# Optimization experiments

Measured on AMD Instinct MI355X. Metric: run time of the kernel, lower is better.

## Reference

```python
import jax, jax.numpy as jnp
import numpy as np

S, L, E = 64, 256, 768          # sentences, tokens per sentence, BERT hidden
N, P = 4096, 32768              # events, event pairs
C, H, D = 256, 4, 64            # CGE channels, heads, head dim (C = H*D = n_last)
M = 8                           # max event span length
MLP_H = 1024
ITERS = 3                       # max_iteration + 1
RATE = 0.5
BETA_INTRA, BETA_INTER = 0.5, 0.5


def setup_inputs():
    key = jax.random.key(0)
    ks = jax.random.split(key, 16)
    nrm = lambda k, shape, sc: jax.random.normal(k, shape, dtype=jnp.float32) * sc
    event_start = jax.random.randint(ks[2], (N,), 0, L - M)
    span = jax.random.randint(ks[3], (N,), 1, M + 1)
    return {
        "sent_emb": nrm(ks[0], (S, L, E), 1.0),
        "proj_in_W": nrm(ks[7], (E, C), E ** -0.5),
        "proj_in_b": jnp.zeros((C,), jnp.float32),
        "proj_W": nrm(ks[8], (C, C), C ** -0.5),
        "proj_b": jnp.zeros((C,), jnp.float32),
        "att_src_intra": nrm(ks[9], (H, D), D ** -0.5),
        "att_dst_intra": nrm(ks[10], (H, D), D ** -0.5),
        "att_src_inter": nrm(ks[11], (H, D), D ** -0.5),
        "att_dst_inter": nrm(ks[12], (H, D), D ** -0.5),
        "mlp_W1": nrm(ks[13], (C + 2 * E, MLP_H), (C + 2 * E) ** -0.5),
        "mlp_b1": jnp.zeros((MLP_H,), jnp.float32),
        "mlp_W2": nrm(ks[14], (MLP_H, 3), MLP_H ** -0.5),
        "mlp_b2": jnp.zeros((3,), jnp.float32),
        "event_sent": jax.random.randint(ks[1], (N,), 0, S),
        "event_start": event_start,
        "event_end": event_start + span,
        "pair_idx": jax.random.randint(ks[4], (P, 2), 0, N),
        "rel_type": jax.random.randint(ks[5], (P,), 0, 2),
        "target": jax.random.randint(ks[6], (P,), 0, 3),
    }


def _attend(h, src, dst, emask, att_src, att_dst):
    # h: [N,H,D]. Masked graph attention, softmax over incoming edges per dst.
    a = jax.nn.leaky_relu((h[src] * att_src).sum(-1) + (h[dst] * att_dst).sum(-1), 0.2)  # [En,H]
    a = jnp.where(emask[:, None], a, -1e9)
    amax = jnp.maximum(jax.ops.segment_max(a, dst, num_segments=N), -1e9)  # [N,H]
    ex = jnp.exp(a - amax[dst]) * emask[:, None].astype(a.dtype)
    denom = jax.ops.segment_sum(ex, dst, num_segments=N)
    alpha = ex / (denom[dst] + 1e-9)
    out = jax.ops.segment_sum(alpha[:, :, None] * h[src], dst, num_segments=N)  # [N,H,D]
    return out.reshape(N, H * D)


def _forward(sent_emb, proj_in_W, proj_in_b, proj_W, proj_b,
             att_src_intra, att_dst_intra, att_src_inter, att_dst_inter,
             mlp_W1, mlp_b1, mlp_W2, mlp_b2,
             event_sent, event_start, event_end, pair_idx, rel_type, target):
    # extract_event: mean of sentence token embeddings over each event span
    pos = event_start[:, None] + jnp.arange(M)                      # [N,M]
    vmask = (pos < event_end[:, None]).astype(sent_emb.dtype)       # [N,M]
    tok = sent_emb[event_sent[:, None], jnp.clip(pos, 0, L - 1)]    # [N,M,E]
    e_emb = (tok * vmask[..., None]).sum(1) / (event_end - event_start).astype(sent_emb.dtype)[:, None]

    p0, p1 = pair_idx[:, 0], pair_idx[:, 1]
    pair_emb = jnp.concatenate([e_emb[p0], e_emb[p1]], axis=-1)     # [P,2E]
    x = e_emb @ proj_in_W + proj_in_b                               # [N,C]

    self_idx = jnp.arange(N)
    ones_n = jnp.ones((N,), bool)
    src_all = jnp.concatenate([p0, p1])
    dst_all = jnp.concatenate([p1, p0])
    intra2 = jnp.concatenate([rel_type == 0, rel_type == 0])

    loss = jnp.float32(0.0)
    pred = None
    for it in range(ITERS):
        diff = x[p0] - x[p1]                                        # [P,C]
        pre = jnp.concatenate([pair_emb, diff], axis=-1)            # [P,2E+C]
        pred = jax.nn.relu(pre @ mlp_W1 + mlp_b1) @ mlp_W2 + mlp_b2  # [P,3]
        logp = jax.nn.log_softmax(pred, axis=-1)
        loss = loss + (1.0 / (it + 1)) * (-jnp.take_along_axis(logp, target[:, None], axis=1).mean())

        # data-dependent edge construction (masked, fixed-size edge lists)
        psoft = jax.nn.softmax(pred, axis=-1)
        conf = psoft.max(1) > RATE
        parg = psoft.argmax(1)
        m_all = jnp.concatenate([conf & (parg == 1), conf & (parg == 2)])

        h = (x @ proj_W + proj_b).reshape(N, H, D)
        # intra edges + always-on self loops
        src_i = jnp.concatenate([src_all, self_idx])
        dst_i = jnp.concatenate([dst_all, self_idx])
        m_i = jnp.concatenate([m_all & intra2, ones_n])
        out_intra = _attend(h, src_i, dst_i, m_i, att_src_intra, att_dst_intra)
        out_inter = _attend(h, src_all, dst_all, m_all & (~intra2), att_src_inter, att_dst_inter)
        x = BETA_INTRA * out_intra + BETA_INTER * out_inter
    return loss, pred


def reference(sent_emb, proj_in_W, proj_in_b, proj_W, proj_b,
              att_src_intra, att_dst_intra, att_src_inter, att_dst_inter,
              mlp_W1, mlp_b1, mlp_W2, mlp_b2,
              event_sent, event_start, event_end, pair_idx, rel_type, target):
    return _forward(sent_emb, proj_in_W, proj_in_b, proj_W, proj_b,
                    att_src_intra, att_dst_intra, att_src_inter, att_dst_inter,
                    mlp_W1, mlp_b1, mlp_W2, mlp_b2,
                    event_sent, event_start, event_end, pair_idx, rel_type, target)
```

## Files before the change

kernel.cpp:

```cpp
#include <hip/hip_runtime.h>
#include <cstddef>
#include <cstdint>

#define NEV   4096
#define NPAIR 32768
#define NEDGE (2*NPAIR)
#define EDIM  768
#define CDIM  256
#define MLPH  1024
#define LLEN  256

typedef unsigned short u16;
typedef __attribute__((ext_vector_type(8))) short bhalf8;
typedef __attribute__((ext_vector_type(4))) float f32x4;

#define GLOAD_LDS(g, l) __builtin_amdgcn_global_load_lds( \
    (const __attribute__((address_space(1))) unsigned int*)(g), \
    (__attribute__((address_space(3))) unsigned int*)(l), 16, 0, 0)

__device__ inline u16 f2bf(float f) {
  union { float f; unsigned u; } v; v.f = f;
  unsigned r = v.u + 0x7fffu + ((v.u >> 16) & 1u);
  return (u16)(r >> 16);
}
__device__ inline float bf2f(u16 h) {
  union { unsigned u; float f; } v; v.u = ((unsigned)h) << 16; return v.f;
}

__global__ void k_zero(int* __restrict__ deg, int* __restrict__ pdeg,
                       float* __restrict__ out) {
  int i = blockIdx.x * 256 + threadIdx.x;
  if (i < NEV) { deg[i] = 0; pdeg[i] = 0; }
  if (i == 0) out[0] = 0.f;
}

__global__ void k_embed(const float* __restrict__ sent, const int* __restrict__ es,
                        const int* __restrict__ st, const int* __restrict__ en,
                        u16* __restrict__ Ahat) {
  int node = blockIdx.x;
  int s = es[node];
  int a = st[node];
  int span = en[node] - a;
  float fspan = (float)span;
  const float* base = sent + ((size_t)s * LLEN + a) * EDIM;
  for (int d = threadIdx.x; d < EDIM; d += 256) {
    float acc = 0.f;
    for (int m = 0; m < span; ++m) acc += base[(size_t)m * EDIM + d];
    float e = acc / fspan;
    u16 hi = f2bf(e);
    float lo = e - bf2f(hi);
    size_t b = (size_t)node * (3 * EDIM);
    Ahat[b + d] = hi;
    Ahat[b + EDIM + d] = hi;
    Ahat[b + 2 * EDIM + d] = f2bf(lo);
  }
}

__global__ void k_count(const int* __restrict__ pair, int* __restrict__ deg) {
  int e = blockIdx.x * 256 + threadIdx.x;
  if (e >= NEDGE) return;
  int p = (e < NPAIR) ? e : e - NPAIR;
  int dst = (e < NPAIR) ? pair[2 * p + 1] : pair[2 * p];
  atomicAdd(&deg[dst], 1);
}

__global__ void k_scan(const int* __restrict__ deg, int* __restrict__ rowp,
                       int* __restrict__ cursor) {
  __shared__ int part[256];
  int t = threadIdx.x;
  int base = t * 16;
  int sum = 0;
  for (int i = 0; i < 16; ++i) sum += deg[base + i];
  part[t] = sum;
  __syncthreads();
  for (int off = 1; off < 256; off <<= 1) {
    int v = (t >= off) ? part[t - off] : 0;
    __syncthreads();
    part[t] += v;
    __syncthreads();
  }
  int run = (t == 0) ? 0 : part[t - 1];
  for (int i = 0; i < 16; ++i) {
    rowp[base + i] = run;
    cursor[base + i] = 0;
    run += deg[base + i];
  }
  if (t == 255) rowp[NEV] = run;
}

__global__ void k_scatter(const int* __restrict__ pair, const int* __restrict__ rowp,
                          int* __restrict__ cursor, int* __restrict__ e_src,
                          int* __restrict__ e_id) {
  int e = blockIdx.x * 256 + threadIdx.x;
  if (e >= NEDGE) return;
  int p   = (e < NPAIR) ? e : e - NPAIR;
  int src = (e < NPAIR) ? pair[2 * p]     : pair[2 * p + 1];
  int dst = (e < NPAIR) ? pair[2 * p + 1] : pair[2 * p];
  int pos = rowp[dst] + atomicAdd(&cursor[dst], 1);
  e_src[pos] = src;
  e_id[pos]  = e;
}

__global__ void k_pcount(const int* __restrict__ pair, int* __restrict__ pdeg) {
  int p = blockIdx.x * 256 + threadIdx.x;
  if (p >= NPAIR) return;
  atomicAdd(&pdeg[pair[2 * p]], 1);
}

__global__ void k_pscatter(const int* __restrict__ pair, const int* __restrict__ prow,
                           int* __restrict__ pcur, int* __restrict__ pidx) {
  int p = blockIdx.x * 256 + threadIdx.x;
  if (p >= NPAIR) return;
  int pos = prow[pair[2 * p]] + atomicAdd(&pcur[pair[2 * p]], 1);
  pidx[pos] = p;
}

__global__ __launch_bounds__(256) void cvt_w(const float* __restrict__ W1,
                                             const float* __restrict__ piW,
                                             const float* __restrict__ projW,
                                             u16* __restrict__ BT, int which)
{
  __shared__ float tile[32][33];
  int K = which ? CDIM : EDIM;
  int ld = K * 3;
  int bk = blockIdx.y * 32;
  int bc = blockIdx.x * 32;
  int tx = threadIdx.x & 31, ty = threadIdx.x >> 5;
#pragma unroll
  for (int rr = 0; rr < 4; ++rr) {
    int k = bk + ty + rr * 8;
    int c = bc + tx;
    float v;
    if (which == 0) {
      v = (c < 1024) ? W1[(size_t)k * MLPH + c]
        : (c < 2048) ? W1[(size_t)(EDIM + k) * MLPH + (c - 1024)]
        : piW[(size_t)k * CDIM + (c - 2048)];
    } else {
      v = (c < 1024) ? W1[(size_t)(2 * EDIM + k) * MLPH + c]
        : projW[(size_t)k * CDIM + (c - 1024)];
    }
    tile[ty + rr * 8][tx] = v;
  }
  __syncthreads();
#pragma unroll
  for (int rr = 0; rr < 4; ++rr) {
    int c = bc + ty + rr * 8;
    int k = bk + tx;
    float v = tile[tx][ty + rr * 8];
    u16 hi = f2bf(v);
    float lo = v - bf2f(hi);
    size_t b = (size_t)c * ld;
    BT[b + k] = hi;
    BT[b + K + k] = f2bf(lo);
    BT[b + 2 * K + k] = hi;
  }
}

__global__ __launch_bounds__(256) void mgemm(
    const u16* __restrict__ A, const u16* __restrict__ BT, int Kp, int mode,
    float* __restrict__ G1, float* __restrict__ G2, u16* __restrict__ Xhat,
    const float* __restrict__ pib, const float* __restrict__ b1,
    const float* __restrict__ pb, float* __restrict__ U, float* __restrict__ V,
    float* __restrict__ h)
{
  __shared__ u16 As[64 * 64];
  __shared__ u16 Bs[64 * 64];
  int tid = threadIdx.x;
  int wave = tid >> 6, lane = tid & 63;

  int gx = gridDim.x;
  int nwg = gx * gridDim.y;
  int orig = blockIdx.y * gx + blockIdx.x;
  int swz = (orig & 7) * (nwg >> 3) + (orig >> 3);
  int bm = (swz / gx) * 64, bn = (swz % gx) * 64;

  int wm = (wave >> 1) * 32, wn = (wave & 1) * 32;

  int srow = tid >> 3;
  int scol = (tid & 7) << 3;
  const u16* Ag = A + (size_t)(bm + srow) * Kp + scol;
  const u16* Bg = BT + (size_t)(bn + srow) * Kp + scol;
  u16* Asd = &As[tid * 8];
  u16* Bsd = &Bs[tid * 8];

  f32x4 acc[2][2];
#pragma unroll
  for (int i = 0; i < 2; ++i)
#pragma unroll
    for (int j = 0; j < 2; ++j) {
      f32x4 z = {0.f, 0.f, 0.f, 0.f};
      acc[i][j] = z;
    }

  int fr = lane & 15;
  int fq = lane >> 4;

  for (int k0 = 0; k0 < Kp; k0 += 64) {
#pragma unroll
    for (int c = 0; c < 2; ++c) {
      GLOAD_LDS(Ag + (size_t)(c * 32) * Kp, Asd + c * 2048);
      GLOAD_LDS(Bg + (size_t)(c * 32) * Kp, Bsd + c * 2048);
    }
    __syncthreads();
#pragma unroll
    for (int kk = 0; kk < 2; ++kk) {
      bhalf8 af[2], bf[2];
#pragma unroll
      for (int i = 0; i < 2; ++i)
        af[i] = *(const bhalf8*)&As[(wm + i * 16 + fr) * 64 + kk * 32 + fq * 8];
#pragma unroll
      for (int j = 0; j < 2; ++j)
        bf[j] = *(const bhalf8*)&Bs[(wn + j * 16 + fr) * 64 + kk * 32 + fq * 8];
#pragma unroll
      for (int i = 0; i < 2; ++i)
#pragma unroll
        for (int j = 0; j < 2; ++j)
          acc[i][j] = __builtin_amdgcn_mfma_f32_16x16x32_bf16(af[i], bf[j], acc[i][j], 0, 0, 0);
    }
    __syncthreads();
    Ag += 64;
    Bg += 64;
  }

#pragma unroll
  for (int i = 0; i < 2; ++i) {
    int mrow = bm + wm + i * 16 + fq * 4;
#pragma unroll
    for (int g = 0; g < 4; ++g) {
      int m = mrow + g;
#pragma unroll
      for (int j = 0; j < 2; ++j) {
        int c = bn + wn + j * 16 + fr;
        float vv = acc[i][j][g];
        if (mode == 0) {
          if (c < 1024) {
            G1[(size_t)m * MLPH + c] = vv;
          } else if (c < 2048) {
            G2[(size_t)m * MLPH + (c - 1024)] = vv;
          } else {
            int cc = c - 2048;
            float xv = vv + pib[cc];
            u16 hi = f2bf(xv);
            float lo = xv - bf2f(hi);
            size_t b = (size_t)m * (3 * CDIM);
            Xhat[b + cc] = hi;
            Xhat[b + CDIM + cc] = hi;
            Xhat[b + 2 * CDIM + cc] = f2bf(lo);
          }
        } else {
          if (c < 1024) {
            size_t idx = (size_t)m * MLPH + c;
            U[idx] = G1[idx] + vv + b1[c];
            V[idx] = G2[idx] - vv;
          } else {
            int cc = c - 1024;
            h[(size_t)m * CDIM + cc] = vv + pb[cc];
          }
        }
      }
    }
  }
}

__global__ void k_s(const float* __restrict__ h,
                    const float* __restrict__ asi, const float* __restrict__ adi,
                    const float* __restrict__ asj, const float* __restrict__ adj,
                    float* __restrict__ sv) {
  int node = blockIdx.x * 4 + (threadIdx.x >> 6);
  int lane = threadIdx.x & 63;
  int head = lane >> 4;
  int d0 = (lane & 15) << 2;
  float4 hv = *(const float4*)(h + (size_t)node * CDIM + head * 64 + d0);
  float4 w1 = *(const float4*)(asi + head * 64 + d0);
  float4 w2 = *(const float4*)(adi + head * 64 + d0);
  float4 w3 = *(const float4*)(asj + head * 64 + d0);
  float4 w4 = *(const float4*)(adj + head * 64 + d0);
  float p1 = hv.x * w1.x + hv.y * w1.y + hv.z * w1.z + hv.w * w1.w;
  float p2 = hv.x * w2.x + hv.y * w2.y + hv.z * w2.z + hv.w * w2.w;
  float p3 = hv.x * w3.x + hv.y * w3.y + hv.z * w3.z + hv.w * w3.w;
  float p4 = hv.x * w4.x + hv.y * w4.y + hv.z * w4.z + hv.w * w4.w;
#pragma unroll
  for (int m = 1; m < 16; m <<= 1) {
    p1 += __shfl_xor(p1, m);
    p2 += __shfl_xor(p2, m);
    p3 += __shfl_xor(p3, m);
    p4 += __shfl_xor(p4, m);
  }
  if ((lane & 15) == 0) {
    sv[0 * NEV * 4 + node * 4 + head] = p1;
    sv[1 * NEV * 4 + node * 4 + head] = p2;
    sv[2 * NEV * 4 + node * 4 + head] = p3;
    sv[3 * NEV * 4 + node * 4 + head] = p4;
  }
}

__global__ __launch_bounds__(256) void k_pred_g(
    const float* __restrict__ U, const float* __restrict__ V,
    const int* __restrict__ pair, const int* __restrict__ prow,
    const int* __restrict__ pidx, const float* __restrict__ W2,
    const float* __restrict__ b2, const int* __restrict__ target,
    int* __restrict__ mstate, float* __restrict__ out,
    float* __restrict__ partials, float lossCoef)
{
  __shared__ float ush[MLPH];
  __shared__ float red[4];
  int n = blockIdx.x;
  int tid = threadIdx.x;
  const float* u = U + (size_t)n * MLPH;
#pragma unroll
  for (int i = 0; i < 4; ++i) ush[tid + i * 256] = u[tid + i * 256];
  __syncthreads();
  int wv = tid >> 6, lane = tid & 63;
  int beg = prow[n], end = prow[n + 1];
  float lsum = 0.f;
  for (int ip = beg + wv; ip < end; ip += 4) {
    int p = pidx[ip];
    int i1 = pair[2 * p + 1];
    const float* v = V + (size_t)i1 * MLPH;
    float a0 = 0.f, a1 = 0.f, a2 = 0.f;
    for (int kb = (lane << 2); kb < MLPH; kb += 256) {
      float4 uu = *(const float4*)(&ush[kb]);
      float4 vv = *(const float4*)(v + kb);
      float h0 = fmaxf(uu.x + vv.x, 0.f);
      float h1 = fmaxf(uu.y + vv.y, 0.f);
      float h2 = fmaxf(uu.z + vv.z, 0.f);
      float h3 = fmaxf(uu.w + vv.w, 0.f);
      const float4* w4 = (const float4*)(W2 + 3 * kb);
      float4 wa = w4[0], wb = w4[1], wc = w4[2];
      a0 += h0 * wa.x + h1 * wa.w + h2 * wb.z + h3 * wc.y;
      a1 += h0 * wa.y + h1 * wb.x + h2 * wb.w + h3 * wc.z;
      a2 += h0 * wa.z + h1 * wb.y + h2 * wc.x + h3 * wc.w;
    }
#pragma unroll
    for (int m = 32; m >= 1; m >>= 1) {
      a0 += __shfl_down(a0, m);
      a1 += __shfl_down(a1, m);
      a2 += __shfl_down(a2, m);
    }
    if (lane == 0) {
      a0 += b2[0]; a1 += b2[1]; a2 += b2[2];
      float mx = fmaxf(a0, fmaxf(a1, a2));
      float e0 = expf(a0 - mx), e1 = expf(a1 - mx), e2 = expf(a2 - mx);
      float sum = e0 + e1 + e2;
      int arg = 0; float best = e0;
      if (e1 > best) { best = e1; arg = 1; }
      if (e2 > best) { best = e2; arg = 2; }
      bool conf = (best / sum) > 0.5f;
      mstate[p] = conf ? arg : -1;
      int t = target[p];
      float predt = (t == 0) ? a0 : ((t == 1) ? a1 : a2);
      float logp = (predt - mx) - logf(sum);
      lsum += -logp * lossCoef;
      float* po = out + 1 + (size_t)p * 3;
      po[0] = a0; po[1] = a1; po[2] = a2;
    }
  }
  if (lane == 0) red[wv] = lsum;
  __syncthreads();
  if (tid == 0) partials[n] = red[0] + red[1] + red[2] + red[3];
}

__global__ void k_lossred(const float* __restrict__ partials, float* __restrict__ out, int n) {
  __shared__ float sm[256];
  float s = 0.f;
  for (int i = threadIdx.x; i < n; i += 256) s += partials[i];
  sm[threadIdx.x] = s;
  __syncthreads();
  for (int off = 128; off; off >>= 1) {
    if (threadIdx.x < off) sm[threadIdx.x] += sm[threadIdx.x + off];
    __syncthreads();
  }
  if (threadIdx.x == 0) out[0] += sm[0];
}

__global__ __launch_bounds__(256) void k_attn(
    const float* __restrict__ h, const float* __restrict__ sv,
    const int* __restrict__ rowp, const int* __restrict__ e_src,
    const int* __restrict__ e_id, const int* __restrict__ mstate,
    const int* __restrict__ rel, u16* __restrict__ Xhat)
{
  int node = blockIdx.x;
  int t = threadIdx.x;
  int head = t >> 6;
  const float* s_si = sv;
  const float* s_di = sv + NEV * 4;
  const float* s_sj = sv + 2 * NEV * 4;
  const float* s_dj = sv + 3 * NEV * 4;
  float sdi = s_di[node * 4 + head];
  float sdj = s_dj[node * 4 + head];
  int beg = rowp[node], end = rowp[node + 1];
  float aself = s_si[node * 4 + head] + sdi;
  aself = aself > 0.f ? aself : 0.2f * aself;
  float mxi = aself;
  float mxj = -1e9f;
  for (int e = beg; e < end; ++e) {
    int eid = e_id[e];
    int pp = (eid < NPAIR) ? eid : eid - NPAIR;
    int st = mstate[pp];
    bool mall = (eid < NPAIR) ? (st == 1) : (st == 2);
    if (!mall) continue;
    int src = e_src[e];
    if (rel[pp] == 0) {
      float a = s_si[src * 4 + head] + sdi;
      a = a > 0.f ? a : 0.2f * a;
      mxi = fmaxf(mxi, a);
    } else {
      float a = s_sj[src * 4 + head] + sdj;
      a = a > 0.f ? a : 0.2f * a;
      mxj = fmaxf(mxj, a);
    }
  }
  float deni = 0.f, denj = 0.f, acci = 0.f, accj = 0.f;
  {
    float ex = expf(aself - mxi);
    deni += ex;
    acci += ex * h[(size_t)node * CDIM + t];
  }
  for (int e = beg; e < end; ++e) {
    int eid = e_id[e];
    int pp = (eid < NPAIR) ? eid : eid - NPAIR;
    int st = mstate[pp];
    bool mall = (eid < NPAIR) ? (st == 1) : (st == 2);
    if (!mall) continue;
    int src = e_src[e];
    float hval = h[(size_t)src * CDIM + t];
    if (rel[pp] == 0) {
      float a = s_si[src * 4 + head] + sdi;
      a = a > 0.f ? a : 0.2f * a;
      float ex = expf(a - mxi);
      deni += ex; acci += ex * hval;
    } else {
      float a = s_sj[src * 4 + head] + sdj;
      a = a > 0.f ? a : 0.2f * a;
      float ex = expf(a - mxj);
      denj += ex; accj += ex * hval;
    }
  }
  float outv = 0.5f * (acci / (deni + 1e-9f)) + 0.5f * (accj / (denj + 1e-9f));
  u16 hi = f2bf(outv);
  float lo = outv - bf2f(hi);
  size_t b = (size_t)node * (3 * CDIM);
  Xhat[b + t] = hi;
  Xhat[b + CDIM + t] = hi;
  Xhat[b + 2 * CDIM + t] = f2bf(lo);
}

extern "C" void kernel_launch(void* const* d_in, const int* in_sizes, int n_in,
                              void* d_out, int out_size, void* d_ws, size_t ws_size,
                              hipStream_t stream)
{
  const float* sent      = (const float*)d_in[0];
  const float* proj_in_W = (const float*)d_in[1];
  const float* proj_in_b = (const float*)d_in[2];
  const float* proj_W    = (const float*)d_in[3];
  const float* proj_b    = (const float*)d_in[4];
  const float* asi       = (const float*)d_in[5];
  const float* adi       = (const float*)d_in[6];
  const float* asj       = (const float*)d_in[7];
  const float* adj       = (const float*)d_in[8];
  const float* W1        = (const float*)d_in[9];
  const float* b1        = (const float*)d_in[10];
  const float* W2        = (const float*)d_in[11];
  const float* b2        = (const float*)d_in[12];
  const int*   es        = (const int*)d_in[13];
  const int*   st        = (const int*)d_in[14];
  const int*   en        = (const int*)d_in[15];
  const int*   pair      = (const int*)d_in[16];
  const int*   rel       = (const int*)d_in[17];
  const int*   target    = (const int*)d_in[18];
  float* out = (float*)d_out;

  char* w = (char*)d_ws;
  auto alloc = [&](size_t bytes) -> char* {
    char* p = w;
    w += (bytes + 255) & ~(size_t)255;
    return p;
  };
  u16*   Ahat = (u16*)alloc(sizeof(u16) * (size_t)NEV * 3 * EDIM);
  u16*   BTe  = (u16*)alloc(sizeof(u16) * (size_t)2304 * 2304);
  u16*   BTu  = (u16*)alloc(sizeof(u16) * (size_t)1280 * 768);
  u16*   Xhat = (u16*)alloc(sizeof(u16) * (size_t)NEV * 3 * CDIM);
  float* G1   = (float*)alloc(sizeof(float) * (size_t)NEV * MLPH);
  float* G2   = (float*)alloc(sizeof(float) * (size_t)NEV * MLPH);
  float* U    = (float*)alloc(sizeof(float) * (size_t)NEV * MLPH);
  float* V    = (float*)alloc(sizeof(float) * (size_t)NEV * MLPH);
  float* h    = (float*)alloc(sizeof(float) * (size_t)NEV * CDIM);
  float* sv   = (float*)alloc(sizeof(float) * (size_t)NEV * 16);
  float* lpart= (float*)alloc(sizeof(float) * NEV);
  int* deg    = (int*)alloc(sizeof(int) * NEV);
  int* rowp   = (int*)alloc(sizeof(int) * (NEV + 1));
  int* cursor = (int*)alloc(sizeof(int) * NEV);
  int* e_src  = (int*)alloc(sizeof(int) * NEDGE);
  int* e_id   = (int*)alloc(sizeof(int) * NEDGE);
  int* pdeg   = (int*)alloc(sizeof(int) * NEV);
  int* prow   = (int*)alloc(sizeof(int) * (NEV + 1));
  int* pcur   = (int*)alloc(sizeof(int) * NEV);
  int* pidx   = (int*)alloc(sizeof(int) * NPAIR);
  int* mstate = (int*)alloc(sizeof(int) * NPAIR);

  k_zero<<<(NEV + 255) / 256, 256, 0, stream>>>(deg, pdeg, out);
  k_embed<<<NEV, 256, 0, stream>>>(sent, es, st, en, Ahat);
  k_count<<<NEDGE / 256, 256, 0, stream>>>(pair, deg);
  k_scan<<<1, 256, 0, stream>>>(deg, rowp, cursor);
  k_scatter<<<NEDGE / 256, 256, 0, stream>>>(pair, rowp, cursor, e_src, e_id);
  k_pcount<<<NPAIR / 256, 256, 0, stream>>>(pair, pdeg);
  k_scan<<<1, 256, 0, stream>>>(pdeg, prow, pcur);
  k_pscatter<<<NPAIR / 256, 256, 0, stream>>>(pair, prow, pcur, pidx);

  cvt_w<<<dim3(2304 / 32, 768 / 32), 256, 0, stream>>>(W1, proj_in_W, proj_W, BTe, 0);
  cvt_w<<<dim3(1280 / 32, 256 / 32), 256, 0, stream>>>(W1, proj_in_W, proj_W, BTu, 1);

  mgemm<<<dim3(2304 / 64, NEV / 64), 256, 0, stream>>>(
      Ahat, BTe, 3 * EDIM, 0, G1, G2, Xhat, proj_in_b,
      nullptr, nullptr, nullptr, nullptr, nullptr);

  for (int it = 0; it < 3; ++it) {
    mgemm<<<dim3(1280 / 64, NEV / 64), 256, 0, stream>>>(
        Xhat, BTu, 3 * CDIM, 1, G1, G2, nullptr, nullptr,
        b1, proj_b, U, V, h);
    k_s<<<NEV / 4, 256, 0, stream>>>(h, asi, adi, asj, adj, sv);
    float coef = 1.0f / ((float)(it + 1) * (float)NPAIR);
    k_pred_g<<<NEV, 256, 0, stream>>>(U, V, pair, prow, pidx, W2, b2, target,
                                      mstate, out, lpart, coef);
    k_lossred<<<1, 256, 0, stream>>>(lpart, out, NEV);
    k_attn<<<NEV, 256, 0, stream>>>(h, sv, rowp, e_src, e_id, mstate, rel, Xhat);
  }
  (void)in_sizes; (void)n_in; (void)out_size; (void)ws_size;
}
```

Baseline: 574.6 us.

## Fuse setup kernels, widen GEMM tile to 128 columns, fold attention scores into epilogue

```diff
diff --git a/kernel.cpp b/kernel.cpp
--- a/kernel.cpp
+++ b/kernel.cpp
@@ -56,17 +56,18 @@
   }
 }
 
-__global__ void k_count(const int* __restrict__ pair, int* __restrict__ deg) {
+__global__ void k_countF(const int* __restrict__ pair, int* __restrict__ deg,
+                         int* __restrict__ pdeg) {
   int e = blockIdx.x * 256 + threadIdx.x;
   if (e >= NEDGE) return;
   int p = (e < NPAIR) ? e : e - NPAIR;
   int dst = (e < NPAIR) ? pair[2 * p + 1] : pair[2 * p];
   atomicAdd(&deg[dst], 1);
-}
-
-__global__ void k_scan(const int* __restrict__ deg, int* __restrict__ rowp,
-                       int* __restrict__ cursor) {
-  __shared__ int part[256];
+  if (e < NPAIR) atomicAdd(&pdeg[pair[2 * e]], 1);
+}
+
+__device__ inline void scan_body(const int* __restrict__ deg, int* __restrict__ rowp,
+                                 int* __restrict__ cursor, int* part) {
   int t = threadIdx.x;
   int base = t * 16;
   int sum = 0;
@@ -88,9 +89,19 @@
   if (t == 255) rowp[NEV] = run;
 }
 
-__global__ void k_scatter(const int* __restrict__ pair, const int* __restrict__ rowp,
-                          int* __restrict__ cursor, int* __restrict__ e_src,
-                          int* __restrict__ e_id) {
+__global__ void k_scanF(const int* __restrict__ deg, int* __restrict__ rowp,
+                        int* __restrict__ cursor, const int* __restrict__ pdeg,
+                        int* __restrict__ prow, int* __restrict__ pcur) {
+  __shared__ int part[256];
+  scan_body(deg, rowp, cursor, part);
+  __syncthreads();
+  scan_body(pdeg, prow, pcur, part);
+}
+
+__global__ void k_scatterF(const int* __restrict__ pair, const int* __restrict__ rowp,
+                           int* __restrict__ cursor, int* __restrict__ e_src,
+                           int* __restrict__ e_id, const int* __restrict__ prow,
+                           int* __restrict__ pcur, int* __restrict__ pidx) {
   int e = blockIdx.x * 256 + threadIdx.x;
   if (e >= NEDGE) return;
   int p   = (e < NPAIR) ? e : e - NPAIR;
@@ -99,31 +110,25 @@
   int pos = rowp[dst] + atomicAdd(&cursor[dst], 1);
   e_src[pos] = src;
   e_id[pos]  = e;
-}
-
-__global__ void k_pcount(const int* __restrict__ pair, int* __restrict__ pdeg) {
-  int p = blockIdx.x * 256 + threadIdx.x;
-  if (p >= NPAIR) return;
-  atomicAdd(&pdeg[pair[2 * p]], 1);
-}
-
-__global__ void k_pscatter(const int* __restrict__ pair, const int* __restrict__ prow,
-                           int* __restrict__ pcur, int* __restrict__ pidx) {
-  int p = blockIdx.x * 256 + threadIdx.x;
-  if (p >= NPAIR) return;
-  int pos = prow[pair[2 * p]] + atomicAdd(&pcur[pair[2 * p]], 1);
-  pidx[pos] = p;
+  if (e < NPAIR) {
+    int pp = prow[pair[2 * e]] + atomicAdd(&pcur[pair[2 * e]], 1);
+    pidx[pp] = e;
+  }
 }
 
 __global__ __launch_bounds__(256) void cvt_w(const float* __restrict__ W1,
                                              const float* __restrict__ piW,
                                              const float* __restrict__ projW,
-                                             u16* __restrict__ BT, int which)
+                                             u16* __restrict__ BTe,
+                                             u16* __restrict__ BTu)
 {
   __shared__ float tile[32][33];
+  int which = (blockIdx.y >= 24) ? 1 : 0;
+  if (which && blockIdx.x >= 40) return;
+  u16* BT = which ? BTu : BTe;
   int K = which ? CDIM : EDIM;
   int ld = K * 3;
-  int bk = blockIdx.y * 32;
+  int bk = (which ? (blockIdx.y - 24) : blockIdx.y) * 32;
   int bc = blockIdx.x * 32;
   int tx = threadIdx.x & 31, ty = threadIdx.x >> 5;
 #pragma unroll
@@ -161,10 +166,12 @@
     float* __restrict__ G1, float* __restrict__ G2, u16* __restrict__ Xhat,
     const float* __restrict__ pib, const float* __restrict__ b1,
     const float* __restrict__ pb, float* __restrict__ U, float* __restrict__ V,
-    float* __restrict__ h)
+    float* __restrict__ h, const float* __restrict__ asi,
+    const float* __restrict__ adi, const float* __restrict__ asj,
+    const float* __restrict__ adj, float* __restrict__ sv)
 {
   __shared__ u16 As[64 * 64];
-  __shared__ u16 Bs[64 * 64];
+  __shared__ u16 Bs[128 * 64];
   int tid = threadIdx.x;
   int wave = tid >> 6, lane = tid & 63;
 
@@ -172,9 +179,9 @@
   int nwg = gx * gridDim.y;
   int orig = blockIdx.y * gx + blockIdx.x;
   int swz = (orig & 7) * (nwg >> 3) + (orig >> 3);
-  int bm = (swz / gx) * 64, bn = (swz % gx) * 64;
-
-  int wm = (wave >> 1) * 32, wn = (wave & 1) * 32;
+  int bm = (swz / gx) * 64, bn = (swz % gx) * 128;
+
+  int wm = (wave >> 1) * 32, wn = (wave & 1) * 64;
 
   int srow = tid >> 3;
   int scol = (tid & 7) << 3;
@@ -183,11 +190,11 @@
   u16* Asd = &As[tid * 8];
   u16* Bsd = &Bs[tid * 8];
 
-  f32x4 acc[2][2];
+  f32x4 acc[2][4];
 #pragma unroll
   for (int i = 0; i < 2; ++i)
 #pragma unroll
-    for (int j = 0; j < 2; ++j) {
+    for (int j = 0; j < 4; ++j) {
       f32x4 z = {0.f, 0.f, 0.f, 0.f};
       acc[i][j] = z;
     }
@@ -197,24 +204,25 @@
 
   for (int k0 = 0; k0 < Kp; k0 += 64) {
 #pragma unroll
-    for (int c = 0; c < 2; ++c) {
+    for (int c = 0; c < 2; ++c)
       GLOAD_LDS(Ag + (size_t)(c * 32) * Kp, Asd + c * 2048);
+#pragma unroll
+    for (int c = 0; c < 4; ++c)
       GLOAD_LDS(Bg + (size_t)(c * 32) * Kp, Bsd + c * 2048);
-    }
     __syncthreads();
 #pragma unroll
     for (int kk = 0; kk < 2; ++kk) {
-      bhalf8 af[2], bf[2];
+      bhalf8 af[2], bf[4];
 #pragma unroll
       for (int i = 0; i < 2; ++i)
         af[i] = *(const bhalf8*)&As[(wm + i * 16 + fr) * 64 + kk * 32 + fq * 8];
 #pragma unroll
-      for (int j = 0; j < 2; ++j)
+      for (int j = 0; j < 4; ++j)
         bf[j] = *(const bhalf8*)&Bs[(wn + j * 16 + fr) * 64 + kk * 32 + fq * 8];
 #pragma unroll
       for (int i = 0; i < 2; ++i)
 #pragma unroll
-        for (int j = 0; j < 2; ++j)
+        for (int j = 0; j < 4; ++j)
           acc[i][j] = __builtin_amdgcn_mfma_f32_16x16x32_bf16(af[i], bf[j], acc[i][j], 0, 0, 0);
     }
     __syncthreads();
@@ -229,7 +237,7 @@
     for (int g = 0; g < 4; ++g) {
       int m = mrow + g;
 #pragma unroll
-      for (int j = 0; j < 2; ++j) {
+      for (int j = 0; j < 4; ++j) {
         int c = bn + wn + j * 16 + fr;
         float vv = acc[i][j][g];
         if (mode == 0) {
@@ -260,37 +268,40 @@
       }
     }
   }
-}
-
-__global__ void k_s(const float* __restrict__ h,
-                    const float* __restrict__ asi, const float* __restrict__ adi,
-                    const float* __restrict__ asj, const float* __restrict__ adj,
-                    float* __restrict__ sv) {
-  int node = blockIdx.x * 4 + (threadIdx.x >> 6);
-  int lane = threadIdx.x & 63;
-  int head = lane >> 4;
-  int d0 = (lane & 15) << 2;
-  float4 hv = *(const float4*)(h + (size_t)node * CDIM + head * 64 + d0);
-  float4 w1 = *(const float4*)(asi + head * 64 + d0);
-  float4 w2 = *(const float4*)(adi + head * 64 + d0);
-  float4 w3 = *(const float4*)(asj + head * 64 + d0);
-  float4 w4 = *(const float4*)(adj + head * 64 + d0);
-  float p1 = hv.x * w1.x + hv.y * w1.y + hv.z * w1.z + hv.w * w1.w;
-  float p2 = hv.x * w2.x + hv.y * w2.y + hv.z * w2.z + hv.w * w2.w;
-  float p3 = hv.x * w3.x + hv.y * w3.y + hv.z * w3.z + hv.w * w3.w;
-  float p4 = hv.x * w4.x + hv.y * w4.y + hv.z * w4.z + hv.w * w4.w;
-#pragma unroll
-  for (int m = 1; m < 16; m <<= 1) {
-    p1 += __shfl_xor(p1, m);
-    p2 += __shfl_xor(p2, m);
-    p3 += __shfl_xor(p3, m);
-    p4 += __shfl_xor(p4, m);
-  }
-  if ((lane & 15) == 0) {
-    sv[0 * NEV * 4 + node * 4 + head] = p1;
-    sv[1 * NEV * 4 + node * 4 + head] = p2;
-    sv[2 * NEV * 4 + node * 4 + head] = p3;
-    sv[3 * NEV * 4 + node * 4 + head] = p4;
+
+  if (mode == 1 && bn >= MLPH) {
+    int hbase = bn - MLPH + wn;
+    int head = hbase >> 6;
+#pragma unroll
+    for (int i = 0; i < 2; ++i) {
+#pragma unroll
+      for (int g = 0; g < 4; ++g) {
+        int m = bm + wm + i * 16 + fq * 4 + g;
+        float p0 = 0.f, p1 = 0.f, p2 = 0.f, p3 = 0.f;
+#pragma unroll
+        for (int j = 0; j < 4; ++j) {
+          int hc = hbase + j * 16 + fr;
+          float hv = acc[i][j][g] + pb[hc];
+          p0 += hv * asi[hc];
+          p1 += hv * adi[hc];
+          p2 += hv * asj[hc];
+          p3 += hv * adj[hc];
+        }
+#pragma unroll
+        for (int mm = 1; mm < 16; mm <<= 1) {
+          p0 += __shfl_xor(p0, mm);
+          p1 += __shfl_xor(p1, mm);
+          p2 += __shfl_xor(p2, mm);
+          p3 += __shfl_xor(p3, mm);
+        }
+        if (fr == 0) {
+          sv[0 * NEV * 4 + m * 4 + head] = p0;
+          sv[1 * NEV * 4 + m * 4 + head] = p1;
+          sv[2 * NEV * 4 + m * 4 + head] = p2;
+          sv[3 * NEV * 4 + m * 4 + head] = p3;
+        }
+      }
+    }
   }
 }
 
@@ -360,24 +371,12 @@
   if (tid == 0) partials[n] = red[0] + red[1] + red[2] + red[3];
 }
 
-__global__ void k_lossred(const float* __restrict__ partials, float* __restrict__ out, int n) {
-  __shared__ float sm[256];
-  float s = 0.f;
-  for (int i = threadIdx.x; i < n; i += 256) s += partials[i];
-  sm[threadIdx.x] = s;
-  __syncthreads();
-  for (int off = 128; off; off >>= 1) {
-    if (threadIdx.x < off) sm[threadIdx.x] += sm[threadIdx.x + off];
-    __syncthreads();
-  }
-  if (threadIdx.x == 0) out[0] += sm[0];
-}
-
 __global__ __launch_bounds__(256) void k_attn(
     const float* __restrict__ h, const float* __restrict__ sv,
     const int* __restrict__ rowp, const int* __restrict__ e_src,
     const int* __restrict__ e_id, const int* __restrict__ mstate,
-    const int* __restrict__ rel, u16* __restrict__ Xhat)
+    const int* __restrict__ rel, u16* __restrict__ Xhat,
+    const float* __restrict__ lpart, float* __restrict__ out)
 {
   int node = blockIdx.x;
   int t = threadIdx.x;
@@ -443,6 +442,19 @@
   Xhat[b + t] = hi;
   Xhat[b + CDIM + t] = hi;
   Xhat[b + 2 * CDIM + t] = f2bf(lo);
+
+  if (blockIdx.x == 0) {
+    __shared__ float sm[256];
+    float s = 0.f;
+    for (int i = t; i < NEV; i += 256) s += lpart[i];
+    sm[t] = s;
+    __syncthreads();
+    for (int off = 128; off; off >>= 1) {
+      if (t < off) sm[t] += sm[t + off];
+      __syncthreads();
+    }
+    if (t == 0) out[0] += sm[0];
+  }
 }
 
 extern "C" void kernel_launch(void* const* d_in, const int* in_sizes, int n_in,
@@ -500,30 +512,26 @@
 
   k_zero<<<(NEV + 255) / 256, 256, 0, stream>>>(deg, pdeg, out);
   k_embed<<<NEV, 256, 0, stream>>>(sent, es, st, en, Ahat);
-  k_count<<<NEDGE / 256, 256, 0, stream>>>(pair, deg);
-  k_scan<<<1, 256, 0, stream>>>(deg, rowp, cursor);
-  k_scatter<<<NEDGE / 256, 256, 0, stream>>>(pair, rowp, cursor, e_src, e_id);
-  k_pcount<<<NPAIR / 256, 256, 0, stream>>>(pair, pdeg);
-  k_scan<<<1, 256, 0, stream>>>(pdeg, prow, pcur);
-  k_pscatter<<<NPAIR / 256, 256, 0, stream>>>(pair, prow, pcur, pidx);
-
-  cvt_w<<<dim3(2304 / 32, 768 / 32), 256, 0, stream>>>(W1, proj_in_W, proj_W, BTe, 0);
-  cvt_w<<<dim3(1280 / 32, 256 / 32), 256, 0, stream>>>(W1, proj_in_W, proj_W, BTu, 1);
-
-  mgemm<<<dim3(2304 / 64, NEV / 64), 256, 0, stream>>>(
+  k_countF<<<NEDGE / 256, 256, 0, stream>>>(pair, deg, pdeg);
+  k_scanF<<<1, 256, 0, stream>>>(deg, rowp, cursor, pdeg, prow, pcur);
+  k_scatterF<<<NEDGE / 256, 256, 0, stream>>>(pair, rowp, cursor, e_src, e_id,
+                                              prow, pcur, pidx);
+  cvt_w<<<dim3(72, 32), 256, 0, stream>>>(W1, proj_in_W, proj_W, BTe, BTu);
+
+  mgemm<<<dim3(2304 / 128, NEV / 64), 256, 0, stream>>>(
       Ahat, BTe, 3 * EDIM, 0, G1, G2, Xhat, proj_in_b,
+      nullptr, nullptr, nullptr, nullptr, nullptr,
       nullptr, nullptr, nullptr, nullptr, nullptr);
 
   for (int it = 0; it < 3; ++it) {
-    mgemm<<<dim3(1280 / 64, NEV / 64), 256, 0, stream>>>(
+    mgemm<<<dim3(1280 / 128, NEV / 64), 256, 0, stream>>>(
         Xhat, BTu, 3 * CDIM, 1, G1, G2, nullptr, nullptr,
-        b1, proj_b, U, V, h);
-    k_s<<<NEV / 4, 256, 0, stream>>>(h, asi, adi, asj, adj, sv);
+        b1, proj_b, U, V, h, asi, adi, asj, adj, sv);
     float coef = 1.0f / ((float)(it + 1) * (float)NPAIR);
     k_pred_g<<<NEV, 256, 0, stream>>>(U, V, pair, prow, pidx, W2, b2, target,
                                       mstate, out, lpart, coef);
-    k_lossred<<<1, 256, 0, stream>>>(lpart, out, NEV);
-    k_attn<<<NEV, 256, 0, stream>>>(h, sv, rowp, e_src, e_id, mstate, rel, Xhat);
+    k_attn<<<NEV, 256, 0, stream>>>(h, sv, rowp, e_src, e_id, mstate, rel, Xhat,
+                                    lpart, out);
   }
   (void)in_sizes; (void)n_in; (void)out_size; (void)ws_size;
 }
```

New measurement: 544.3 us. 5.3% less time.
